# Optimization experiments

Measured on AMD Instinct MI355X. Metric: run time of the kernel, lower is better.

## Reference

```python
import jax, jax.numpy as jnp
import numpy as np

T, B, L, I, H = 1024, 1024, 10, 10, 10


def setup_inputs() -> dict:
    key = jax.random.key(0)
    ks = jax.random.split(key, 7)
    scale = 1.0 / np.sqrt(H)
    x = jax.random.normal(ks[0], (T, B, I), dtype=jnp.float32)
    hp = jax.random.normal(ks[1], (L, B, H), dtype=jnp.float32)
    cp = jax.random.normal(ks[2], (L, B, H), dtype=jnp.float32)
    # torch nn.LSTM params, uniform(-1/sqrt(H), 1/sqrt(H)); layer 0 input = I == H so all layers stack
    W_ih = jax.random.uniform(ks[3], (L, 4 * H, I), minval=-scale, maxval=scale, dtype=jnp.float32)
    W_hh = jax.random.uniform(ks[4], (L, 4 * H, H), minval=-scale, maxval=scale, dtype=jnp.float32)
    b_ih = jax.random.uniform(ks[5], (L, 4 * H), minval=-scale, maxval=scale, dtype=jnp.float32)
    b_hh = jax.random.uniform(ks[6], (L, 4 * H), minval=-scale, maxval=scale, dtype=jnp.float32)
    return {"x": x, "hp": hp, "cp": cp, "W_ih": W_ih, "W_hh": W_hh, "b_ih": b_ih, "b_hh": b_hh}


def _run_layer(inp, h0, c0, Wi, Wh, bi, bh):
    # precompute input projections for all timesteps: [T, B, 4H]
    xg = jnp.einsum('tbi,gi->tbg', inp, Wi) + bi + bh

    def step(carry, xg_t):
        h, c = carry
        g = xg_t + h @ Wh.T  # [B, 4H]; torch gate order: i, f, g, o
        i_g, f_g, g_g, o_g = jnp.split(g, 4, axis=-1)
        i_g = jax.nn.sigmoid(i_g)
        f_g = jax.nn.sigmoid(f_g)
        g_g = jnp.tanh(g_g)
        o_g = jax.nn.sigmoid(o_g)
        c = f_g * c + i_g * g_g
        h = o_g * jnp.tanh(c)
        return (h, c), h

    (hT, cT), ys = jax.lax.scan(step, (h0, c0), xg)
    return ys, hT, cT


def reference(x, hp, cp, W_ih, W_hh, b_ih, b_hh):
    out = x
    hns, cns = [], []
    for l in range(hp.shape[0]):  # fixed small layer stack
        out, hn, cn = _run_layer(out, hp[l], cp[l], W_ih[l], W_hh[l], b_ih[l], b_hh[l])
        hns.append(hn)
        cns.append(cn)
    return out, jnp.stack(hns), jnp.stack(cns)
```

## Files before the change

kernel.cpp:

```cpp
#include <hip/hip_runtime.h>

namespace {

constexpr int T = 1024;
constexpr int B = 1024;
constexpr int L = 10;
constexpr int H = 10;
constexpr int NTHREADS = 128;
constexpr int NSTEP = T + L - 1;
constexpr int BH = B * H;

using v2f = __attribute__((ext_vector_type(2))) float;

__device__ __forceinline__ v2f v2fma(v2f a, v2f b, v2f c) {
    return __builtin_elementwise_fma(a, b, c);
}

__device__ __forceinline__ void pin(v2f& v) { asm volatile("" : "+v"(v)); }
__device__ __forceinline__ void pin(float& v) { asm volatile("" : "+v"(v)); }

__device__ __forceinline__ float sigmoid_f(float x) {
    return __builtin_amdgcn_rcpf(1.0f + __expf(-x));
}
__device__ __forceinline__ float tanh_f(float x) {
    return 1.0f - 2.0f * __builtin_amdgcn_rcpf(1.0f + __expf(2.0f * x));
}

__global__
__attribute__((amdgpu_flat_work_group_size(NTHREADS, NTHREADS)))
__attribute__((amdgpu_waves_per_eu(2, 2)))
void lstm_pipeline(const float* __restrict__ x,
                   const float* __restrict__ hp,
                   const float* __restrict__ cp,
                   const float* __restrict__ Wih,
                   const float* __restrict__ Whh,
                   const float* __restrict__ bih,
                   const float* __restrict__ bhh,
                   float* __restrict__ out,
                   float* __restrict__ hn,
                   float* __restrict__ cn)
{
    __shared__ __align__(16) float buf[L + 1][2][12];

    const int tid = threadIdx.x;
    const bool active = tid < L * H;
    const int l = active ? tid / H : L - 1;
    const int j = active ? tid % H : H - 1;
    const int b = blockIdx.x;
    const int boff = b * H + j;

    v2f wi2[4][5], wh2[4][5];
    float bias[4];
    float c = 0.0f, xa = 0.0f;

    if (active) {
        #pragma unroll
        for (int g = 0; g < 4; ++g) {
            const size_t row = (size_t)(l * 4 * H + g * H + j);
            const float* wr = Wih + row * H;
            const float* hr = Whh + row * H;
            #pragma unroll
            for (int p = 0; p < 5; ++p) {
                v2f a; a[0] = wr[2 * p]; a[1] = wr[2 * p + 1]; wi2[g][p] = a;
                v2f d; d[0] = hr[2 * p]; d[1] = hr[2 * p + 1]; wh2[g][p] = d;
            }
            bias[g] = bih[row] + bhh[row];
        }
        #pragma unroll
        for (int g = 0; g < 4; ++g) {
            #pragma unroll
            for (int p = 0; p < 5; ++p) { pin(wi2[g][p]); pin(wh2[g][p]); }
            pin(bias[g]);
        }
        c = cp[(l * B + b) * H + j];
        buf[l + 1][(l & 1) ^ 1][j] = hp[(l * B + b) * H + j];
        if (l == 0) {
            buf[0][1][j] = x[boff];
            xa = x[BH + boff];
        }
    }
    __syncthreads();

    auto step = [&](int s, int wp, int rp) {
        if (active) {
            const int t = s - l;
            if (t >= 0 && t < T) {
                float xin[12], hin[12];
                {
                    float4* xv = (float4*)xin;
                    float4* hv = (float4*)hin;
                    const float4* xs = (const float4*)&buf[l][rp][0];
                    const float4* hs = (const float4*)&buf[l + 1][rp][0];
                    xv[0] = xs[0]; xv[1] = xs[1]; xv[2] = xs[2];
                    hv[0] = hs[0]; hv[1] = hs[1]; hv[2] = hs[2];
                }

                v2f acc2[4];
                #pragma unroll
                for (int g = 0; g < 4; ++g) {
                    v2f a; a[0] = bias[g]; a[1] = 0.0f; acc2[g] = a;
                }
                #pragma unroll
                for (int p = 0; p < 5; ++p) {
                    v2f xp; xp[0] = xin[2 * p]; xp[1] = xin[2 * p + 1];
                    #pragma unroll
                    for (int g = 0; g < 4; ++g) acc2[g] = v2fma(wi2[g][p], xp, acc2[g]);
                }
                #pragma unroll
                for (int p = 0; p < 5; ++p) {
                    v2f hh; hh[0] = hin[2 * p]; hh[1] = hin[2 * p + 1];
                    #pragma unroll
                    for (int g = 0; g < 4; ++g) acc2[g] = v2fma(wh2[g][p], hh, acc2[g]);
                }

                const float ig = sigmoid_f(acc2[0][0] + acc2[0][1]);
                const float fg = sigmoid_f(acc2[1][0] + acc2[1][1]);
                const float gg = tanh_f(acc2[2][0] + acc2[2][1]);
                const float og = sigmoid_f(acc2[3][0] + acc2[3][1]);
                c = fmaf(fg, c, ig * gg);
                const float hval = og * tanh_f(c);

                buf[l + 1][wp][j] = hval;
                if (l == L - 1) {
                    out[(size_t)t * BH + boff] = hval;
                }
            }
            if (l == 0 && (s + 1) < T) {
                buf[0][wp][j] = xa;
                if ((s + 2) < T) xa = x[(size_t)(s + 2) * BH + boff];
            }
        }
        __syncthreads();
    };

    for (int sb = 0; sb < NSTEP + 1; sb += 2) {
        step(sb, 0, 1);
        step(sb + 1, 1, 0);
    }

    if (active) {
        hn[(l * B + b) * H + j] = buf[l + 1][(l + 1) & 1][j];
        cn[(l * B + b) * H + j] = c;
    }
}

}

extern "C" void kernel_launch(void* const* d_in, const int* in_sizes, int n_in,
                              void* d_out, int out_size, void* d_ws, size_t ws_size,
                              hipStream_t stream) {
    (void)in_sizes; (void)n_in; (void)d_ws; (void)ws_size; (void)out_size;
    const float* x   = (const float*)d_in[0];
    const float* hp  = (const float*)d_in[1];
    const float* cp  = (const float*)d_in[2];
    const float* Wih = (const float*)d_in[3];
    const float* Whh = (const float*)d_in[4];
    const float* bih = (const float*)d_in[5];
    const float* bhh = (const float*)d_in[6];

    float* out = (float*)d_out;
    float* hn  = out + (size_t)T * B * H;
    float* cn  = hn + (size_t)L * B * H;

    lstm_pipeline<<<dim3(B), dim3(NTHREADS), 0, stream>>>(
        x, hp, cp, Wih, Whh, bih, bhh, out, hn, cn);
}
```

Measured before the change: 543.3 us.

## Split each LSTM cell across lane pairs with DPP exchange and chunked x prefetch

Each hidden unit now uses two lanes: one computes the input projection, the other the recurrent projection, and they swap partial gate sums, activations and tanh(c) via DPP quad_perm lane swaps. This halves per-thread FMA work and register pressure on the serial critical path, and waves_per_eu is raised to 4 to match 256 threads. The x input for layer 0 is prefetched in chunks of 8 timesteps so the global load latency is hidden over several steps. The cost is redundant activation work on both lanes, extra cross-lane exchanges per step, and more waves taking part in each barrier.

Result: slower. 1.427 ms (+162.7%).

```diff
diff --git a/kernel.cpp b/kernel.cpp
--- a/kernel.cpp
+++ b/kernel.cpp
@@ -6,9 +6,11 @@
 constexpr int B = 1024;
 constexpr int L = 10;
 constexpr int H = 10;
-constexpr int NTHREADS = 128;
+constexpr int NTHREADS = 256;
 constexpr int NSTEP = T + L - 1;
 constexpr int BH = B * H;
+constexpr int CH = 8;
+constexpr int NCHUNK = (NSTEP + CH - 1) / CH;
 
 using v2f = __attribute__((ext_vector_type(2))) float;
 
@@ -16,8 +18,11 @@
     return __builtin_elementwise_fma(a, b, c);
 }
 
-__device__ __forceinline__ void pin(v2f& v) { asm volatile("" : "+v"(v)); }
-__device__ __forceinline__ void pin(float& v) { asm volatile("" : "+v"(v)); }
+__device__ __forceinline__ float lane_swap(float v) {
+    int i = __builtin_bit_cast(int, v);
+    i = __builtin_amdgcn_mov_dpp(i, 0xB1, 0xF, 0xF, true);
+    return __builtin_bit_cast(float, i);
+}
 
 __device__ __forceinline__ float sigmoid_f(float x) {
     return __builtin_amdgcn_rcpf(1.0f + __expf(-x));
@@ -28,7 +33,7 @@
 
 __global__
 __attribute__((amdgpu_flat_work_group_size(NTHREADS, NTHREADS)))
-__attribute__((amdgpu_waves_per_eu(2, 2)))
+__attribute__((amdgpu_waves_per_eu(4, 4)))
 void lstm_pipeline(const float* __restrict__ x,
                    const float* __restrict__ hp,
                    const float* __restrict__ cp,
@@ -43,56 +48,55 @@
     __shared__ __align__(16) float buf[L + 1][2][12];
 
     const int tid = threadIdx.x;
-    const bool active = tid < L * H;
-    const int l = active ? tid / H : L - 1;
-    const int j = active ? tid % H : H - 1;
+    const bool active = tid < L * H * 2;
+    const int l    = active ? tid / (2 * H) : L - 1;
+    const int j    = active ? (tid % (2 * H)) >> 1 : H - 1;
+    const bool hsel = tid & 1;
     const int b = blockIdx.x;
     const int boff = b * H + j;
 
-    v2f wi2[4][5], wh2[4][5];
+    v2f w2[4][5];
     float bias[4];
-    float c = 0.0f, xa = 0.0f;
+    float c = 0.0f;
+    float xcur[CH], xnext[CH];
 
     if (active) {
+        const float* Wsel = hsel ? Whh : Wih;
         #pragma unroll
         for (int g = 0; g < 4; ++g) {
             const size_t row = (size_t)(l * 4 * H + g * H + j);
-            const float* wr = Wih + row * H;
-            const float* hr = Whh + row * H;
+            const float* wr = Wsel + row * H;
             #pragma unroll
             for (int p = 0; p < 5; ++p) {
-                v2f a; a[0] = wr[2 * p]; a[1] = wr[2 * p + 1]; wi2[g][p] = a;
-                v2f d; d[0] = hr[2 * p]; d[1] = hr[2 * p + 1]; wh2[g][p] = d;
+                v2f a; a[0] = wr[2 * p]; a[1] = wr[2 * p + 1]; w2[g][p] = a;
             }
-            bias[g] = bih[row] + bhh[row];
-        }
-        #pragma unroll
-        for (int g = 0; g < 4; ++g) {
-            #pragma unroll
-            for (int p = 0; p < 5; ++p) { pin(wi2[g][p]); pin(wh2[g][p]); }
-            pin(bias[g]);
+            bias[g] = hsel ? 0.0f : (bih[row] + bhh[row]);
         }
         c = cp[(l * B + b) * H + j];
-        buf[l + 1][(l & 1) ^ 1][j] = hp[(l * B + b) * H + j];
-        if (l == 0) {
+        if (hsel) {
+            buf[l + 1][(l & 1) ^ 1][j] = hp[(l * B + b) * H + j];
+        }
+        if (l == 0 && !hsel) {
             buf[0][1][j] = x[boff];
-            xa = x[BH + boff];
+            #pragma unroll
+            for (int i = 0; i < CH; ++i) xcur[i] = x[(size_t)(1 + i) * BH + boff];
         }
     }
+    const float k2 = hsel ? -1.0f : 2.0f;
+    const float A2 = hsel ? 0.0f : 1.0f;
+    const float B2 = hsel ? -1.0f : 2.0f;
     __syncthreads();
 
     auto step = [&](int s, int wp, int rp) {
         if (active) {
             const int t = s - l;
             if (t >= 0 && t < T) {
-                float xin[12], hin[12];
+                float in[12];
                 {
-                    float4* xv = (float4*)xin;
-                    float4* hv = (float4*)hin;
-                    const float4* xs = (const float4*)&buf[l][rp][0];
-                    const float4* hs = (const float4*)&buf[l + 1][rp][0];
-                    xv[0] = xs[0]; xv[1] = xs[1]; xv[2] = xs[2];
-                    hv[0] = hs[0]; hv[1] = hs[1]; hv[2] = hs[2];
+                    float4* iv = (float4*)in;
+                    const float4* src = hsel ? (const float4*)&buf[l + 1][rp][0]
+                                             : (const float4*)&buf[l][rp][0];
+                    iv[0] = src[0]; iv[1] = src[1]; iv[2] = src[2];
                 }
 
                 v2f acc2[4];
@@ -102,43 +106,62 @@
                 }
                 #pragma unroll
                 for (int p = 0; p < 5; ++p) {
-                    v2f xp; xp[0] = xin[2 * p]; xp[1] = xin[2 * p + 1];
+                    v2f ip; ip[0] = in[2 * p]; ip[1] = in[2 * p + 1];
                     #pragma unroll
-                    for (int g = 0; g < 4; ++g) acc2[g] = v2fma(wi2[g][p], xp, acc2[g]);
-                }
-                #pragma unroll
-                for (int p = 0; p < 5; ++p) {
-                    v2f hh; hh[0] = hin[2 * p]; hh[1] = hin[2 * p + 1];
-                    #pragma unroll
-                    for (int g = 0; g < 4; ++g) acc2[g] = v2fma(wh2[g][p], hh, acc2[g]);
+                    for (int g = 0; g < 4; ++g) acc2[g] = v2fma(w2[g][p], ip, acc2[g]);
                 }
 
-                const float ig = sigmoid_f(acc2[0][0] + acc2[0][1]);
-                const float fg = sigmoid_f(acc2[1][0] + acc2[1][1]);
-                const float gg = tanh_f(acc2[2][0] + acc2[2][1]);
-                const float og = sigmoid_f(acc2[3][0] + acc2[3][1]);
-                c = fmaf(fg, c, ig * gg);
-                const float hval = og * tanh_f(c);
+                float p_if = acc2[hsel ? 1 : 0][0] + acc2[hsel ? 1 : 0][1];
+                float p_go = acc2[hsel ? 3 : 2][0] + acc2[hsel ? 3 : 2][1];
+                float s_if = acc2[hsel ? 0 : 1][0] + acc2[hsel ? 0 : 1][1];
+                float s_go = acc2[hsel ? 2 : 3][0] + acc2[hsel ? 2 : 3][1];
+                const float e0 = p_if + lane_swap(s_if);
+                const float e1 = p_go + lane_swap(s_go);
 
-                buf[l + 1][wp][j] = hval;
-                if (l == L - 1) {
-                    out[(size_t)t * BH + boff] = hval;
+                const float s0 = sigmoid_f(e0);
+                const float e  = __expf(k2 * e1);
+                const float v1 = A2 - B2 * __builtin_amdgcn_rcpf(1.0f + e);
+                const float a  = s0 * v1;
+                const float recv_s = lane_swap(s0);
+                c = fmaf(recv_s, c, a);
+                const float tc = tanh_f(c);
+                const float recv_t = lane_swap(tc);
+                const float hval = v1 * recv_t;
+
+                if (hsel) {
+                    buf[l + 1][wp][j] = hval;
+                    if (l == L - 1) out[(size_t)t * BH + boff] = hval;
                 }
             }
-            if (l == 0 && (s + 1) < T) {
-                buf[0][wp][j] = xa;
-                if ((s + 2) < T) xa = x[(size_t)(s + 2) * BH + boff];
+            if (l == 0 && !hsel && (s + 1) < T) {
+                buf[0][wp][j] = xcur[s & (CH - 1)];
             }
         }
         __syncthreads();
     };
 
-    for (int sb = 0; sb < NSTEP + 1; sb += 2) {
-        step(sb, 0, 1);
-        step(sb + 1, 1, 0);
+    for (int k = 0; k < NCHUNK; ++k) {
+        const int s0 = k * CH;
+        if (active && l == 0 && !hsel) {
+            #pragma unroll
+            for (int i = 0; i < CH; ++i) {
+                int t = s0 + CH + 1 + i;
+                t = t < T ? t : T - 1;
+                xnext[i] = x[(size_t)t * BH + boff];
+            }
+        }
+        #pragma unroll
+        for (int u = 0; u < CH; u += 2) {
+            step(s0 + u, 0, 1);
+            step(s0 + u + 1, 1, 0);
+        }
+        if (active && l == 0 && !hsel) {
+            #pragma unroll
+            for (int i = 0; i < CH; ++i) xcur[i] = xnext[i];
+        }
     }
 
-    if (active) {
+    if (active && !hsel) {
         hn[(l * B + b) * H + j] = buf[l + 1][(l + 1) & 1][j];
         cn[(l * B + b) * H + j] = c;
     }
```

## Batch four timesteps per barrier using wave-local hidden-state exchange

Applied to the files above, without the earlier changes.

The layer-wavefront pipeline now advances in windows of four timesteps per block barrier instead of one. Threads are remapped so that each layer's ten threads sit inside a single wavefront, which lets the recurrent h exchange go through a per-layer LDS row without a block barrier. Inter-layer inputs are passed as four-step slabs through a double buffer. This cuts the number of __syncthreads roughly fourfold, at the cost of a longer pipeline fill and drain and a reliance on in-wave LDS ordering. Weights are also staged through LDS before being loaded into registers, and the register pinning is dropped.

After: 509.3 us. 1.07x faster.

```diff
diff --git a/kernel.cpp b/kernel.cpp
--- a/kernel.cpp
+++ b/kernel.cpp
@@ -7,17 +7,17 @@
 constexpr int L = 10;
 constexpr int H = 10;
 constexpr int NTHREADS = 128;
-constexpr int NSTEP = T + L - 1;
+constexpr int U = 4;
+constexpr int NWIN = T / U;
+constexpr int NINT = NWIN + L - 1;
 constexpr int BH = B * H;
+constexpr int WSLOT = 88;
 
 using v2f = __attribute__((ext_vector_type(2))) float;
 
 __device__ __forceinline__ v2f v2fma(v2f a, v2f b, v2f c) {
     return __builtin_elementwise_fma(a, b, c);
 }
-
-__device__ __forceinline__ void pin(v2f& v) { asm volatile("" : "+v"(v)); }
-__device__ __forceinline__ void pin(float& v) { asm volatile("" : "+v"(v)); }
 
 __device__ __forceinline__ float sigmoid_f(float x) {
     return __builtin_amdgcn_rcpf(1.0f + __expf(-x));
@@ -40,106 +40,122 @@
                    float* __restrict__ hn,
                    float* __restrict__ cn)
 {
-    __shared__ __align__(16) float buf[L + 1][2][12];
+    __shared__ __align__(16) float wlds[L * H * WSLOT];
+    __shared__ __align__(16) float buf[L + 1][2][U][12];
+    __shared__ __align__(16) float hbuf[L][12];
 
     const int tid = threadIdx.x;
-    const bool active = tid < L * H;
-    const int l = active ? tid / H : L - 1;
-    const int j = active ? tid % H : H - 1;
+    const int wv = tid >> 6, ln = tid & 63;
+    const bool active = (wv == 0) ? (ln < 60) : (ln < 40);
+    const int lidx = (wv == 0) ? ln : 60 + ln;
+    const int l = active ? lidx / 10 : L - 1;
+    const int j = active ? lidx % 10 : H - 1;
     const int b = blockIdx.x;
     const int boff = b * H + j;
 
-    v2f wi2[4][5], wh2[4][5];
-    float bias[4];
-    float c = 0.0f, xa = 0.0f;
-
     if (active) {
+        float* slot = &wlds[(l * H + j) * WSLOT];
         #pragma unroll
         for (int g = 0; g < 4; ++g) {
             const size_t row = (size_t)(l * 4 * H + g * H + j);
             const float* wr = Wih + row * H;
             const float* hr = Whh + row * H;
             #pragma unroll
-            for (int p = 0; p < 5; ++p) {
-                v2f a; a[0] = wr[2 * p]; a[1] = wr[2 * p + 1]; wi2[g][p] = a;
-                v2f d; d[0] = hr[2 * p]; d[1] = hr[2 * p + 1]; wh2[g][p] = d;
-            }
-            bias[g] = bih[row] + bhh[row];
-        }
-        #pragma unroll
-        for (int g = 0; g < 4; ++g) {
+            for (int i = 0; i < H; ++i) slot[g * H + i] = wr[i];
             #pragma unroll
-            for (int p = 0; p < 5; ++p) { pin(wi2[g][p]); pin(wh2[g][p]); }
-            pin(bias[g]);
-        }
-        c = cp[(l * B + b) * H + j];
-        buf[l + 1][(l & 1) ^ 1][j] = hp[(l * B + b) * H + j];
-        if (l == 0) {
-            buf[0][1][j] = x[boff];
-            xa = x[BH + boff];
+            for (int i = 0; i < H; ++i) slot[40 + g * H + i] = hr[i];
+            slot[80 + g] = bih[row] + bhh[row];
         }
     }
     __syncthreads();
 
-    auto step = [&](int s, int wp, int rp) {
-        if (active) {
-            const int t = s - l;
-            if (t >= 0 && t < T) {
-                float xin[12], hin[12];
+    v2f wi2[4][5], wh2[4][5];
+    float bias[4];
+    {
+        const float* slot = &wlds[(active ? l * H + j : 0) * WSLOT];
+        #pragma unroll
+        for (int g = 0; g < 4; ++g) {
+            #pragma unroll
+            for (int p = 0; p < 5; ++p) {
+                v2f a; a[0] = slot[g * H + 2 * p];      a[1] = slot[g * H + 2 * p + 1];      wi2[g][p] = a;
+                v2f d; d[0] = slot[40 + g * H + 2 * p]; d[1] = slot[40 + g * H + 2 * p + 1]; wh2[g][p] = d;
+            }
+            bias[g] = slot[80 + g];
+        }
+    }
+
+    float h = 0.0f, c = 0.0f;
+    float xcur[U], xnext[U];
+    if (active) {
+        h = hp[(l * B + b) * H + j];
+        c = cp[(l * B + b) * H + j];
+        hbuf[l][j] = h;
+        if (l == 0) {
+            #pragma unroll
+            for (int u = 0; u < U; ++u) buf[0][1][u][j] = x[(size_t)u * BH + boff];
+            #pragma unroll
+            for (int u = 0; u < U; ++u) xcur[u] = x[(size_t)(U + u) * BH + boff];
+        }
+    }
+    __syncthreads();
+
+    for (int k = 0; k < NINT; ++k) {
+        const int wp = k & 1, rp = wp ^ 1;
+        if (active && l == 0 && (k + 2) < NWIN) {
+            #pragma unroll
+            for (int u = 0; u < U; ++u)
+                xnext[u] = x[(size_t)((k + 2) * U + u) * BH + boff];
+        }
+        const unsigned w = (unsigned)(k - l);
+        if (active && w < (unsigned)NWIN) {
+            const int t0 = (int)w * U;
+            #pragma unroll
+            for (int u = 0; u < U; ++u) {
+                float xin[12], hrow[12];
                 {
-                    float4* xv = (float4*)xin;
-                    float4* hv = (float4*)hin;
-                    const float4* xs = (const float4*)&buf[l][rp][0];
-                    const float4* hs = (const float4*)&buf[l + 1][rp][0];
-                    xv[0] = xs[0]; xv[1] = xs[1]; xv[2] = xs[2];
-                    hv[0] = hs[0]; hv[1] = hs[1]; hv[2] = hs[2];
+                    const float4* xs = (const float4*)&buf[l][rp][u][0];
+                    ((float4*)xin)[0] = xs[0]; ((float4*)xin)[1] = xs[1]; ((float4*)xin)[2] = xs[2];
+                    const float4* hs = (const float4*)&hbuf[l][0];
+                    ((float4*)hrow)[0] = hs[0]; ((float4*)hrow)[1] = hs[1]; ((float4*)hrow)[2] = hs[2];
                 }
-
-                v2f acc2[4];
+                v2f acc[4];
                 #pragma unroll
-                for (int g = 0; g < 4; ++g) {
-                    v2f a; a[0] = bias[g]; a[1] = 0.0f; acc2[g] = a;
-                }
+                for (int g = 0; g < 4; ++g) { v2f a; a[0] = bias[g]; a[1] = 0.0f; acc[g] = a; }
                 #pragma unroll
                 for (int p = 0; p < 5; ++p) {
                     v2f xp; xp[0] = xin[2 * p]; xp[1] = xin[2 * p + 1];
                     #pragma unroll
-                    for (int g = 0; g < 4; ++g) acc2[g] = v2fma(wi2[g][p], xp, acc2[g]);
+                    for (int g = 0; g < 4; ++g) acc[g] = v2fma(wi2[g][p], xp, acc[g]);
                 }
                 #pragma unroll
                 for (int p = 0; p < 5; ++p) {
-                    v2f hh; hh[0] = hin[2 * p]; hh[1] = hin[2 * p + 1];
+                    v2f hh; hh[0] = hrow[2 * p]; hh[1] = hrow[2 * p + 1];
                     #pragma unroll
-                    for (int g = 0; g < 4; ++g) acc2[g] = v2fma(wh2[g][p], hh, acc2[g]);
+                    for (int g = 0; g < 4; ++g) acc[g] = v2fma(wh2[g][p], hh, acc[g]);
                 }
+                const float ig = sigmoid_f(acc[0][0] + acc[0][1]);
+                const float fg = sigmoid_f(acc[1][0] + acc[1][1]);
+                const float gg = tanh_f(acc[2][0] + acc[2][1]);
+                const float og = sigmoid_f(acc[3][0] + acc[3][1]);
+                c = fmaf(fg, c, ig * gg);
+                h = og * tanh_f(c);
 
-                const float ig = sigmoid_f(acc2[0][0] + acc2[0][1]);
-                const float fg = sigmoid_f(acc2[1][0] + acc2[1][1]);
-                const float gg = tanh_f(acc2[2][0] + acc2[2][1]);
-                const float og = sigmoid_f(acc2[3][0] + acc2[3][1]);
-                c = fmaf(fg, c, ig * gg);
-                const float hval = og * tanh_f(c);
-
-                buf[l + 1][wp][j] = hval;
-                if (l == L - 1) {
-                    out[(size_t)t * BH + boff] = hval;
-                }
-            }
-            if (l == 0 && (s + 1) < T) {
-                buf[0][wp][j] = xa;
-                if ((s + 2) < T) xa = x[(size_t)(s + 2) * BH + boff];
+                hbuf[l][j] = h;
+                if (l < L - 1) buf[l + 1][wp][u][j] = h;
+                else out[(size_t)(t0 + u) * BH + boff] = h;
             }
         }
+        if (active && l == 0 && (k + 1) < NWIN) {
+            #pragma unroll
+            for (int u = 0; u < U; ++u) buf[0][wp][u][j] = xcur[u];
+            #pragma unroll
+            for (int u = 0; u < U; ++u) xcur[u] = xnext[u];
+        }
         __syncthreads();
-    };
-
-    for (int sb = 0; sb < NSTEP + 1; sb += 2) {
-        step(sb, 0, 1);
-        step(sb + 1, 1, 0);
     }
 
     if (active) {
-        hn[(l * B + b) * H + j] = buf[l + 1][(l + 1) & 1][j];
+        hn[(l * B + b) * H + j] = h;
         cn[(l * B + b) * H + j] = c;
     }
 }
```
